# Kernel tuning notes

Measured on AMD Instinct MI355X. Metric: run time of the kernel, lower is better.

Reference implementation:

```python
import jax, jax.numpy as jnp
import numpy as np

B, T, C = 1, 2048, 1024
H = 16
HD = C // H
BLOCK = 2048
NEG = float('-inf')

def setup_inputs() -> dict:
    key = jax.random.key(0)
    ks = jax.random.split(key, 6)
    x = jax.random.normal(ks[0], (B, T, C), dtype=jnp.float32)
    cumulative_scores = jax.random.normal(ks[1], (B, T), dtype=jnp.float32) * 0.1
    padding_mask = jnp.ones((B, T), dtype=jnp.float32)
    token_index = jax.random.randint(ks[2], (B, T), 0, BLOCK).astype(jnp.int64)
    w_attn = jax.random.normal(ks[3], (C, 3 * C), dtype=jnp.float32) * (1.0 / np.sqrt(C))
    b_attn = jnp.zeros((3 * C,), dtype=jnp.float32)
    w_proj = jax.random.normal(ks[4], (C, C), dtype=jnp.float32) * (1.0 / np.sqrt(C))
    b_proj = jnp.zeros((C,), dtype=jnp.float32)
    return dict(x=x, cumulative_scores=cumulative_scores, padding_mask=padding_mask,
                token_index=token_index, w_attn=w_attn, b_attn=b_attn,
                w_proj=w_proj, b_proj=b_proj)

def _rotate_half(z):
    z1, z2 = z[..., : z.shape[-1] // 2], z[..., z.shape[-1] // 2 :]
    return jnp.concatenate((-z2, z1), axis=-1)

def reference(x, cumulative_scores, padding_mask, token_index, w_attn, b_attn, w_proj, b_proj):
    # fused QKV projection
    qkv = x @ w_attn + b_attn                      # (B,T,3C)
    q, k, v = jnp.split(qkv, 3, axis=2)
    q = q.reshape(B, T, H, HD).transpose(0, 2, 1, 3)  # (B,H,T,HD)
    k = k.reshape(B, T, H, HD).transpose(0, 2, 1, 3)
    v = v.reshape(B, T, H, HD).transpose(0, 2, 1, 3)

    # dynamic per-token RoPE positions: global token counts (original scatter
    # broadcasts indices over batch, so counts are global across all batches)
    cnt = jnp.zeros((BLOCK,), jnp.float32).at[token_index.reshape(-1)].add(1.0)
    per_tok = (1.0 / (cnt + 1e-10))[token_index]       # (B,T)
    partial = jnp.cumsum(per_tok, axis=-1)             # (B,T) fractional positions

    inv_freq = 1.0 / (10000.0 ** (jnp.arange(0, HD, 2, dtype=jnp.float32) / HD))
    freqs = partial[..., None] * inv_freq              # (B,T,HD/2)
    emb = jnp.concatenate((freqs, freqs), axis=-1)     # (B,T,HD)
    cos = jnp.cos(emb)[:, None]                        # (B,1,T,HD)
    sin = jnp.sin(emb)[:, None]
    q = q * cos + _rotate_half(q) * sin
    k = k * cos + _rotate_half(k) * sin

    # 'fork' plan: overwrite last channel
    q = q.at[..., -1].set(1.0)
    k = k.at[..., -1].set(jnp.broadcast_to(cumulative_scores[:, None, :], (B, H, T)))

    # additive causal + padding mask (B,T,T)
    causal = jnp.where(jnp.tril(jnp.ones((T, T), jnp.bool_)), 0.0, NEG)
    pm = jnp.take_along_axis(padding_mask, token_index, axis=1)     # (B,T)
    outer = pm[:, :, None] * pm[:, None, :]
    pad_add = jnp.where(outer.astype(jnp.bool_), 0.0, NEG)
    mask = causal[None, :, :] + pad_add                              # (B,T,T)

    # scale v by exp(cumulative_scores)
    v = v * jnp.exp(cumulative_scores)[:, None, :, None]

    scores = jnp.einsum('bhqd,bhkd->bhqk', q, k) / np.sqrt(HD) + mask[:, None]
    probs = jax.nn.softmax(scores, axis=-1)
    y = jnp.einsum('bhqk,bhkd->bhqd', probs, v)        # (B,H,T,HD)
    y = y.transpose(0, 2, 1, 3).reshape(B, T, C)
    return y @ w_proj + b_proj
```

## Files before the change

### kernel.cpp

```cpp
#include <hip/hip_runtime.h>
#include <math.h>

#define T 2048
#define C 1024
#define H 16
#define HD 64
#define N3 (3*C)
#define NBLOCK 2048

typedef __attribute__((ext_vector_type(8))) short bf16x8;
typedef __attribute__((ext_vector_type(4))) float f32x4;

#define MFMA16(a, b, c) __builtin_amdgcn_mfma_f32_16x16x32_bf16((a), (b), (c), 0, 0, 0)

__device__ inline short f2bf(float f) {
    unsigned u; __builtin_memcpy(&u, &f, 4);
    unsigned r = (u + 0x7fffu + ((u >> 16) & 1u)) >> 16;
    return (short)r;
}
__device__ inline float bf2f(short s) {
    unsigned u = ((unsigned)(unsigned short)s) << 16;
    float f; __builtin_memcpy(&f, &u, 4);
    return f;
}

__device__ inline void gload_lds16(const void* g, void* l) {
    __builtin_amdgcn_global_load_lds((const __attribute__((address_space(1))) unsigned int*)g,
                                     (__attribute__((address_space(3))) unsigned int*)l,
                                     16, 0, 0);
}

__global__ __launch_bounds__(256) void pre_kernel(const float* __restrict__ x,
                                                  const float* __restrict__ w_attn,
                                                  const float* __restrict__ w_proj,
                                                  const int* __restrict__ tok,
                                                  const float* __restrict__ padmask,
                                                  short* __restrict__ xb,
                                                  short* __restrict__ wabT,
                                                  short* __restrict__ wpbT,
                                                  float* __restrict__ partial,
                                                  float* __restrict__ pm_tok) {
    int bid = blockIdx.x;
    int tid = threadIdx.x;
    if (bid == 3072) {
        __shared__ float cntS[NBLOCK];
        __shared__ float sums[256];
        #pragma unroll
        for (int j = 0; j < 8; ++j) cntS[tid * 8 + j] = 0.0f;
        __syncthreads();
        int tk[8];
        #pragma unroll
        for (int j = 0; j < 8; ++j) {
            tk[j] = tok[tid * 8 + j];
            atomicAdd(&cntS[tk[j]], 1.0f);
        }
        __syncthreads();
        float vals[8];
        float s = 0.0f;
        #pragma unroll
        for (int j = 0; j < 8; ++j) {
            s += 1.0f / (cntS[tk[j]] + 1e-10f);
            vals[j] = s;
            pm_tok[tid * 8 + j] = padmask[tk[j]];
        }
        sums[tid] = s;
        __syncthreads();
        for (int off = 1; off < 256; off <<= 1) {
            float v = (tid >= off) ? sums[tid - off] : 0.0f;
            __syncthreads();
            sums[tid] += v;
            __syncthreads();
        }
        float offset = (tid > 0) ? sums[tid - 1] : 0.0f;
        #pragma unroll
        for (int j = 0; j < 8; ++j) partial[tid * 8 + j] = offset + vals[j];
        return;
    }
    if (bid < 2048) {
        int i = bid * 1024 + tid * 4;
        float4 v = *(const float4*)(x + i);
        short4 o;
        o.x = f2bf(v.x); o.y = f2bf(v.y); o.z = f2bf(v.z); o.w = f2bf(v.w);
        *(short4*)(xb + i) = o;
        return;
    }
    __shared__ float S[64][65];
    const float* in; short* out; int Kd, Nd, bx, by;
    if (bid < 2816) {
        int b = bid - 2048;
        bx = b % 48; by = b / 48;
        in = w_attn; out = wabT; Kd = C; Nd = N3;
    } else {
        int b = bid - 2816;
        bx = b % 16; by = b / 16;
        in = w_proj; out = wpbT; Kd = C; Nd = C;
    }
    int n0 = bx * 64, k0 = by * 64;
    #pragma unroll
    for (int i = 0; i < 16; ++i) {
        int lin = tid + i * 256;
        int r = lin >> 6, c = lin & 63;
        S[r][c] = in[(size_t)(k0 + r) * Nd + n0 + c];
    }
    __syncthreads();
    #pragma unroll
    for (int i = 0; i < 16; ++i) {
        int lin = tid + i * 256;
        int rn = lin >> 6, ck = lin & 63;
        out[(size_t)(n0 + rn) * Kd + k0 + ck] = f2bf(S[ck][rn]);
    }
}

template <int OUT_BF16, int EPI>
__global__ __launch_bounds__(256) void gemm_bt64(const short* __restrict__ A,
                                                 const short* __restrict__ Bt,
                                                 const float* __restrict__ bias,
                                                 void* __restrict__ Cout,
                                                 int M, int N, int K,
                                                 const float* __restrict__ partial,
                                                 const float* __restrict__ cumsc,
                                                 const float* __restrict__ pm_tok,
                                                 short* __restrict__ vbT) {
    __shared__ alignas(16) short As[2][64 * 32];
    __shared__ alignas(16) short Bs[2][128 * 32];
    int tid = threadIdx.x;
    int nwg = gridDim.x * gridDim.y;
    int bidl = blockIdx.y * gridDim.x + blockIdx.x;
    int swz = (bidl & 7) * (nwg >> 3) + (bidl >> 3);
    int m0 = (swz / gridDim.x) * 64, n0 = (swz % gridDim.x) * 128;
    int w = tid >> 6, l = tid & 63;
    int wm = (w >> 1) * 32, wn = (w & 1) * 64;
    int lq = l & 15, g = l >> 4;
    int prow = l >> 2, pcol = (l & 3) * 8;
    f32x4 acc[2][4] = {};
    for (int k0 = 0; k0 < K; k0 += 64) {
        #pragma unroll
        for (int hf = 0; hf < 2; ++hf) {
            int kk = k0 + hf * 32;
            int rowA = w * 16 + prow;
            gload_lds16(A + (size_t)(m0 + rowA) * K + kk + pcol, As[hf] + w * 512);
            #pragma unroll
            for (int i = 0; i < 2; ++i) {
                int c = w * 2 + i;
                int row = c * 16 + prow;
                gload_lds16(Bt + (size_t)(n0 + row) * K + kk + pcol, Bs[hf] + c * 512);
            }
        }
        __syncthreads();
        #pragma unroll
        for (int hf = 0; hf < 2; ++hf) {
            bf16x8 af[2], bfr[4];
            #pragma unroll
            for (int f = 0; f < 2; ++f)
                af[f] = *(const bf16x8*)(As[hf] + (wm + f * 16 + lq) * 32 + g * 8);
            #pragma unroll
            for (int j = 0; j < 4; ++j)
                bfr[j] = *(const bf16x8*)(Bs[hf] + (wn + j * 16 + lq) * 32 + g * 8);
            #pragma unroll
            for (int fi = 0; fi < 2; ++fi)
                #pragma unroll
                for (int fj = 0; fj < 4; ++fj)
                    acc[fi][fj] = MFMA16(af[fi], bfr[fj], acc[fi][fj]);
        }
        __syncthreads();
    }

    if (EPI == 0) {
        #pragma unroll
        for (int fi = 0; fi < 2; ++fi)
            #pragma unroll
            for (int fj = 0; fj < 4; ++fj)
                #pragma unroll
                for (int r = 0; r < 4; ++r) {
                    int m = m0 + wm + fi * 16 + g * 4 + r;
                    int n = n0 + wn + fj * 16 + lq;
                    float v = acc[fi][fj][r] + bias[n];
                    if (OUT_BF16) ((short*)Cout)[(size_t)m * N + n] = f2bf(v);
                    else          ((float*)Cout)[(size_t)m * N + n] = v;
                }
    } else {
        short* Cb = (short*)Cout;
        int cb = n0 + wn;
        int section = cb >> 10;
        float b0 = bias[cb + lq],      b1 = bias[cb + 16 + lq];
        float b2 = bias[cb + 32 + lq], b3 = bias[cb + 48 + lq];
        if (section < 2) {
            bool isQ = (section == 0);
            float inv0 = exp2f(-(float)lq * (13.287712379549449f / 32.0f));
            float inv1 = exp2f(-(float)(lq + 16) * (13.287712379549449f / 32.0f));
            #pragma unroll
            for (int fi = 0; fi < 2; ++fi)
                #pragma unroll
                for (int r = 0; r < 4; ++r) {
                    int trow = m0 + wm + fi * 16 + g * 4 + r;
                    float pt = partial[trow];
                    float sn0, cs0, sn1, cs1;
                    __sincosf(pt * inv0, &sn0, &cs0);
                    __sincosf(pt * inv1, &sn1, &cs1);
                    float a0 = acc[fi][0][r] + b0;
                    float a1 = acc[fi][1][r] + b1;
                    float a2 = acc[fi][2][r] + b2;
                    float a3 = acc[fi][3][r] + b3;
                    float lo0 = a0 * cs0 - a2 * sn0;
                    float hi0 = a2 * cs0 + a0 * sn0;
                    float lo1 = a1 * cs1 - a3 * sn1;
                    float hi1 = a3 * cs1 + a1 * sn1;
                    if (lq == 15) {
                        float pm = pm_tok[trow];
                        hi1 = isQ ? ((pm != 0.0f) ? 1.0f : 0.0f)
                                  : ((pm != 0.0f) ? cumsc[trow] : -1e20f);
                    }
                    size_t base = (size_t)trow * N3 + cb;
                    Cb[base + lq]      = f2bf(lo0);
                    Cb[base + 16 + lq] = f2bf(lo1);
                    Cb[base + 32 + lq] = f2bf(hi0);
                    Cb[base + 48 + lq] = f2bf(hi1);
                }
        } else {
            int h = (cb - 2 * C) >> 6;
            #pragma unroll
            for (int fi = 0; fi < 2; ++fi) {
                int tb = m0 + wm + fi * 16 + g * 4;
                float ef[4];
                #pragma unroll
                for (int r = 0; r < 4; ++r) ef[r] = __expf(cumsc[tb + r]);
                #pragma unroll
                for (int fj = 0; fj < 4; ++fj) {
                    int d = fj * 16 + lq;
                    float bv = (fj == 0) ? b0 : (fj == 1) ? b1 : (fj == 2) ? b2 : b3;
                    short4 o;
                    o.x = f2bf((acc[fi][fj][0] + bv) * ef[0]);
                    o.y = f2bf((acc[fi][fj][1] + bv) * ef[1]);
                    o.z = f2bf((acc[fi][fj][2] + bv) * ef[2]);
                    o.w = f2bf((acc[fi][fj][3] + bv) * ef[3]);
                    *(short4*)(vbT + (size_t)(h * 64 + d) * T + tb) = o;
                }
            }
        }
    }
}

__global__ __launch_bounds__(256) void attn_flash(const short* __restrict__ qkvb,
                                                  const short* __restrict__ vbT,
                                                  short* __restrict__ yb) {
    __shared__ alignas(16) short Kt[2][64 * 64];
    __shared__ alignas(16) short Vt[2][64 * 64];
    __shared__ alignas(16) short Ps[4][16][72];

    int b = blockIdx.x;
    int h, qt;
    if (b < 256) { h = b & 15; qt = 31 - (b >> 4); }
    else         { int c2 = b - 256; h = c2 & 15; qt = c2 >> 4; }
    int tid = threadIdx.x;
    int w = tid >> 6, l = tid & 63;
    int lq = l & 15, g = l >> 4;
    int qrl = w * 16 + lq;

    const short* qbase = qkvb + (size_t)(qt * 64 + qrl) * N3 + h * 64;
    bf16x8 qf0 = *(const bf16x8*)(qbase + g * 8);
    bf16x8 qf1 = *(const bf16x8*)(qbase + 32 + g * 8);

    f32x4 accO[4] = {};
    float lsum = 0.0f;

    int srow = tid >> 3, scol = (tid & 7) * 8;
    const short* kgb = qkvb + C + h * 64 + scol;
    const short* vgb = vbT + (size_t)(h * 64) * T + scol;
    int wb0 = srow * 128 + ((scol * 2) ^ ((srow & 7) << 4));
    int wb1 = (srow + 32) * 128 + ((scol * 2) ^ ((srow & 7) << 4));

    auto do_tile = [&](int cur, bool masked) {
        const char* Kc = (const char*)Kt[cur];
        const char* Vc = (const char*)Vt[cur];
        f32x4 s[4] = {};
        __builtin_amdgcn_s_setprio(1);
        #pragma unroll
        for (int f = 0; f < 4; ++f) {
            int row = f * 16 + lq;
            const char* kr_ = Kc + row * 128;
            int sw = (row & 7) << 4;
            bf16x8 a0 = *(const bf16x8*)(kr_ + ((g * 16) ^ sw));
            bf16x8 a1 = *(const bf16x8*)(kr_ + ((64 + g * 16) ^ sw));
            s[f] = MFMA16(a0, qf0, s[f]);
            s[f] = MFMA16(a1, qf1, s[f]);
        }
        __builtin_amdgcn_s_setprio(0);
        float p[16];
        #pragma unroll
        for (int f = 0; f < 4; ++f)
            #pragma unroll
            for (int r = 0; r < 4; ++r) {
                float sv = s[f][r] * 0.125f;
                if (masked) {
                    int kl = f * 16 + g * 4 + r;
                    sv = (kl > qrl) ? -INFINITY : sv;
                }
                float pv = __expf(sv);
                p[f * 4 + r] = pv;
                lsum += pv;
            }
        #pragma unroll
        for (int f = 0; f < 4; ++f) {
            unsigned u0, u1;
            asm("v_cvt_pk_bf16_f32 %0, %1, %2" : "=v"(u0) : "v"(p[f * 4 + 0]), "v"(p[f * 4 + 1]));
            asm("v_cvt_pk_bf16_f32 %0, %1, %2" : "=v"(u1) : "v"(p[f * 4 + 2]), "v"(p[f * 4 + 3]));
            uint2 uu; uu.x = u0; uu.y = u1;
            *(uint2*)&Ps[w][lq][f * 16 + g * 4] = uu;
        }
        __builtin_amdgcn_s_setprio(1);
        #pragma unroll
        for (int kh = 0; kh < 2; ++kh) {
            bf16x8 pa = *(const bf16x8*)&Ps[w][lq][kh * 32 + g * 8];
            #pragma unroll
            for (int f = 0; f < 4; ++f) {
                int vrow = f * 16 + lq;
                const char* vr_ = Vc + vrow * 128;
                bf16x8 vb = *(const bf16x8*)(vr_ + (((kh * 32 + g * 8) * 2) ^ ((vrow & 7) << 4)));
                accO[f] = MFMA16(pa, vb, accO[f]);
            }
        }
        __builtin_amdgcn_s_setprio(0);
    };

    uint4 kr0 = *(const uint4*)(kgb + (size_t)srow * N3);
    uint4 kr1 = *(const uint4*)(kgb + (size_t)(srow + 32) * N3);
    uint4 vr0 = *(const uint4*)(vgb + (size_t)srow * T);
    uint4 vr1 = *(const uint4*)(vgb + (size_t)(srow + 32) * T);
    *(uint4*)((char*)Kt[0] + wb0) = kr0;
    *(uint4*)((char*)Kt[0] + wb1) = kr1;
    *(uint4*)((char*)Vt[0] + wb0) = vr0;
    *(uint4*)((char*)Vt[0] + wb1) = vr1;
    __syncthreads();

    for (int t = 0; t < qt; ++t) {
        int kn = (t + 1) * 64;
        kr0 = *(const uint4*)(kgb + (size_t)(kn + srow) * N3);
        kr1 = *(const uint4*)(kgb + (size_t)(kn + srow + 32) * N3);
        vr0 = *(const uint4*)(vgb + (size_t)srow * T + kn);
        vr1 = *(const uint4*)(vgb + (size_t)(srow + 32) * T + kn);

        do_tile(t & 1, false);

        int nxt = (t & 1) ^ 1;
        *(uint4*)((char*)Kt[nxt] + wb0) = kr0;
        *(uint4*)((char*)Kt[nxt] + wb1) = kr1;
        *(uint4*)((char*)Vt[nxt] + wb0) = vr0;
        *(uint4*)((char*)Vt[nxt] + wb1) = vr1;
        __syncthreads();
    }
    do_tile(qt & 1, true);

    lsum += __shfl_xor(lsum, 16);
    lsum += __shfl_xor(lsum, 32);
    float linv_own = 1.0f / lsum;
    float li[4];
    #pragma unroll
    for (int r = 0; r < 4; ++r) li[r] = __shfl(linv_own, g * 4 + r);

    #pragma unroll
    for (int f = 0; f < 4; ++f)
        #pragma unroll
        for (int r = 0; r < 4; ++r) {
            int trow = qt * 64 + w * 16 + g * 4 + r;
            yb[(size_t)trow * C + h * 64 + f * 16 + lq] = f2bf(accO[f][r] * li[r]);
        }
}

extern "C" void kernel_launch(void* const* d_in, const int* in_sizes, int n_in,
                              void* d_out, int out_size, void* d_ws, size_t ws_size,
                              hipStream_t stream) {
    const float* x       = (const float*)d_in[0];
    const float* cumsc   = (const float*)d_in[1];
    const float* padmask = (const float*)d_in[2];
    const int*   tok     = (const int*)d_in[3];
    const float* w_attn  = (const float*)d_in[4];
    const float* b_attn  = (const float*)d_in[5];
    const float* w_proj  = (const float*)d_in[6];
    const float* b_proj  = (const float*)d_in[7];
    float* out = (float*)d_out;

    float* part   = (float*)d_ws;
    float* pm_tok = part + 2048;
    short* xb     = (short*)(pm_tok + 2048);
    short* wabT   = xb + (size_t)T * C;
    short* wpbT   = wabT + (size_t)N3 * C;
    short* qkvb   = wpbT + (size_t)C * C;
    short* vbT    = qkvb + (size_t)T * N3;
    short* yb     = vbT + (size_t)C * T;

    pre_kernel<<<3073, 256, 0, stream>>>(x, w_attn, w_proj, tok, padmask,
                                         xb, wabT, wpbT, part, pm_tok);
    gemm_bt64<1, 1><<<dim3(N3 / 128, T / 64), 256, 0, stream>>>(
        xb, wabT, b_attn, qkvb, T, N3, C, part, cumsc, pm_tok, vbT);
    attn_flash<<<512, 256, 0, stream>>>(qkvb, vbT, yb);
    gemm_bt64<0, 0><<<dim3(C / 128, T / 64), 256, 0, stream>>>(
        yb, wpbT, b_proj, out, T, C, C, nullptr, nullptr, nullptr, nullptr);
}
```

Baseline: 83.29 us.

## Split long causal attention rows across two blocks and combine partials

Query tiles 16-31 now have their key range split into two blocks (tiles 0-16 and 17-qt). Each half writes unnormalized fp32 partial outputs and row sums to workspace, and a new combine kernel adds them, normalizes, and writes bf16. This balances per-block work under the causal mask and raises block count from 512 to 768. The cost is an extra kernel launch plus fp32 partial writes and reads. The split relies on there being no running max, which matches the existing unnormalized softmax.

```diff
diff --git a/kernel.cpp b/kernel.cpp
--- a/kernel.cpp
+++ b/kernel.cpp
@@ -242,21 +242,27 @@
 
 __global__ __launch_bounds__(256) void attn_flash(const short* __restrict__ qkvb,
                                                   const short* __restrict__ vbT,
-                                                  short* __restrict__ yb) {
+                                                  short* __restrict__ yb,
+                                                  float* __restrict__ Opart,
+                                                  float* __restrict__ Lpart) {
     __shared__ alignas(16) short Kt[2][64 * 64];
     __shared__ alignas(16) short Vt[2][64 * 64];
     __shared__ alignas(16) short Ps[4][16][72];
 
     int b = blockIdx.x;
-    int h, qt;
-    if (b < 256) { h = b & 15; qt = 31 - (b >> 4); }
-    else         { int c2 = b - 256; h = c2 & 15; qt = c2 >> 4; }
+    int h, qt, t0, t1, mode;
+    if (b < 256)      { h = b & 15; qt = 16 + (b >> 4); t0 = 0;  t1 = 16; mode = 1; }
+    else if (b < 512) { int c = b - 256; h = c & 15; qt = 31 - (c >> 4); t0 = 17; t1 = qt; mode = 2; }
+    else              { int c = b - 512; h = c & 15; qt = c >> 4; t0 = 0; t1 = qt; mode = 0; }
+    int nt = t1 - t0 + 1;
+
     int tid = threadIdx.x;
     int w = tid >> 6, l = tid & 63;
     int lq = l & 15, g = l >> 4;
     int qrl = w * 16 + lq;
-
-    const short* qbase = qkvb + (size_t)(qt * 64 + qrl) * N3 + h * 64;
+    int qrow = qt * 64 + qrl;
+
+    const short* qbase = qkvb + (size_t)qrow * N3 + h * 64;
     bf16x8 qf0 = *(const bf16x8*)(qbase + g * 8);
     bf16x8 qf1 = *(const bf16x8*)(qbase + 32 + g * 8);
 
@@ -269,9 +275,24 @@
     int wb0 = srow * 128 + ((scol * 2) ^ ((srow & 7) << 4));
     int wb1 = (srow + 32) * 128 + ((scol * 2) ^ ((srow & 7) << 4));
 
-    auto do_tile = [&](int cur, bool masked) {
-        const char* Kc = (const char*)Kt[cur];
-        const char* Vc = (const char*)Vt[cur];
+    uint4 kr0, kr1, vr0, vr1;
+    auto stageRegs = [&](int tile) {
+        int kb = tile * 64;
+        kr0 = *(const uint4*)(kgb + (size_t)(kb + srow) * N3);
+        kr1 = *(const uint4*)(kgb + (size_t)(kb + srow + 32) * N3);
+        vr0 = *(const uint4*)(vgb + (size_t)srow * T + kb);
+        vr1 = *(const uint4*)(vgb + (size_t)(srow + 32) * T + kb);
+    };
+    auto writeLds = [&](int buf) {
+        *(uint4*)((char*)Kt[buf] + wb0) = kr0;
+        *(uint4*)((char*)Kt[buf] + wb1) = kr1;
+        *(uint4*)((char*)Vt[buf] + wb0) = vr0;
+        *(uint4*)((char*)Vt[buf] + wb1) = vr1;
+    };
+
+    auto do_tile = [&](int buf, bool masked) {
+        const char* Kc = (const char*)Kt[buf];
+        const char* Vc = (const char*)Vt[buf];
         f32x4 s[4] = {};
         __builtin_amdgcn_s_setprio(1);
         #pragma unroll
@@ -322,48 +343,74 @@
         __builtin_amdgcn_s_setprio(0);
     };
 
-    uint4 kr0 = *(const uint4*)(kgb + (size_t)srow * N3);
-    uint4 kr1 = *(const uint4*)(kgb + (size_t)(srow + 32) * N3);
-    uint4 vr0 = *(const uint4*)(vgb + (size_t)srow * T);
-    uint4 vr1 = *(const uint4*)(vgb + (size_t)(srow + 32) * T);
-    *(uint4*)((char*)Kt[0] + wb0) = kr0;
-    *(uint4*)((char*)Kt[0] + wb1) = kr1;
-    *(uint4*)((char*)Vt[0] + wb0) = vr0;
-    *(uint4*)((char*)Vt[0] + wb1) = vr1;
+    if (nt > 0) { stageRegs(t0); writeLds(0); }
     __syncthreads();
 
-    for (int t = 0; t < qt; ++t) {
-        int kn = (t + 1) * 64;
-        kr0 = *(const uint4*)(kgb + (size_t)(kn + srow) * N3);
-        kr1 = *(const uint4*)(kgb + (size_t)(kn + srow + 32) * N3);
-        vr0 = *(const uint4*)(vgb + (size_t)srow * T + kn);
-        vr1 = *(const uint4*)(vgb + (size_t)(srow + 32) * T + kn);
-
-        do_tile(t & 1, false);
-
-        int nxt = (t & 1) ^ 1;
-        *(uint4*)((char*)Kt[nxt] + wb0) = kr0;
-        *(uint4*)((char*)Kt[nxt] + wb1) = kr1;
-        *(uint4*)((char*)Vt[nxt] + wb0) = vr0;
-        *(uint4*)((char*)Vt[nxt] + wb1) = vr1;
-        __syncthreads();
-    }
-    do_tile(qt & 1, true);
+    for (int j = 0; j < nt; ++j) {
+        int t = t0 + j;
+        bool pf = (j + 1 < nt);
+        if (pf) stageRegs(t + 1);
+        do_tile(j & 1, t == qt);
+        if (pf) writeLds((j & 1) ^ 1);
+        __syncthreads();
+    }
 
     lsum += __shfl_xor(lsum, 16);
     lsum += __shfl_xor(lsum, 32);
-    float linv_own = 1.0f / lsum;
-    float li[4];
+
+    if (mode == 0) {
+        float linv_own = 1.0f / lsum;
+        float li[4];
+        #pragma unroll
+        for (int r = 0; r < 4; ++r) li[r] = __shfl(linv_own, g * 4 + r);
+        #pragma unroll
+        for (int f = 0; f < 4; ++f)
+            #pragma unroll
+            for (int r = 0; r < 4; ++r) {
+                int trow = qt * 64 + w * 16 + g * 4 + r;
+                yb[(size_t)trow * C + h * 64 + f * 16 + lq] = f2bf(accO[f][r] * li[r]);
+            }
+    } else {
+        int kh = mode - 1;
+        int slab = h * 16 + (qt - 16);
+        float* Ob = Opart + ((size_t)kh * 256 + slab) * 4096;
+        #pragma unroll
+        for (int f = 0; f < 4; ++f)
+            #pragma unroll
+            for (int r = 0; r < 4; ++r)
+                Ob[(w * 16 + g * 4 + r) * 64 + f * 16 + lq] = accO[f][r];
+        if (g == 0) Lpart[((size_t)kh * 256 + slab) * 64 + w * 16 + lq] = lsum;
+    }
+}
+
+__global__ __launch_bounds__(256) void attn_combine(const float* __restrict__ Opart,
+                                                    const float* __restrict__ Lpart,
+                                                    short* __restrict__ yb) {
+    __shared__ float linvS[64];
+    int s = blockIdx.x;
+    int h = s >> 4, qt = 16 + (s & 15);
+    int tid = threadIdx.x;
+    if (tid < 64)
+        linvS[tid] = 1.0f / (Lpart[(size_t)s * 64 + tid] + Lpart[(size_t)(256 + s) * 64 + tid]);
+    __syncthreads();
+    const float* O0 = Opart + (size_t)s * 4096;
+    const float* O1 = Opart + (size_t)(256 + s) * 4096;
     #pragma unroll
-    for (int r = 0; r < 4; ++r) li[r] = __shfl(linv_own, g * 4 + r);
-
-    #pragma unroll
-    for (int f = 0; f < 4; ++f)
-        #pragma unroll
-        for (int r = 0; r < 4; ++r) {
-            int trow = qt * 64 + w * 16 + g * 4 + r;
-            yb[(size_t)trow * C + h * 64 + f * 16 + lq] = f2bf(accO[f][r] * li[r]);
-        }
+    for (int e = 0; e < 4; ++e) {
+        int idx = (tid * 4 + e * 1024);
+        int base = tid * 4 + e * 1024;
+        float4 a = *(const float4*)(O0 + base);
+        float4 c = *(const float4*)(O1 + base);
+        int q = base >> 6, d = base & 63;
+        float li = linvS[q];
+        short4 o;
+        o.x = f2bf((a.x + c.x) * li);
+        o.y = f2bf((a.y + c.y) * li);
+        o.z = f2bf((a.z + c.z) * li);
+        o.w = f2bf((a.w + c.w) * li);
+        *(short4*)(yb + (size_t)(qt * 64 + q) * C + h * 64 + d) = o;
+        (void)idx;
+    }
 }
 
 extern "C" void kernel_launch(void* const* d_in, const int* in_sizes, int n_in,
@@ -381,7 +428,9 @@
 
     float* part   = (float*)d_ws;
     float* pm_tok = part + 2048;
-    short* xb     = (short*)(pm_tok + 2048);
+    float* Opart  = pm_tok + 2048;
+    float* Lpart  = Opart + (size_t)2 * 256 * 4096;
+    short* xb     = (short*)(Lpart + 2 * 256 * 64);
     short* wabT   = xb + (size_t)T * C;
     short* wpbT   = wabT + (size_t)N3 * C;
     short* qkvb   = wpbT + (size_t)C * C;
@@ -392,7 +441,8 @@
                                          xb, wabT, wpbT, part, pm_tok);
     gemm_bt64<1, 1><<<dim3(N3 / 128, T / 64), 256, 0, stream>>>(
         xb, wabT, b_attn, qkvb, T, N3, C, part, cumsc, pm_tok, vbT);
-    attn_flash<<<512, 256, 0, stream>>>(qkvb, vbT, yb);
+    attn_flash<<<768, 256, 0, stream>>>(qkvb, vbT, yb, Opart, Lpart);
+    attn_combine<<<256, 256, 0, stream>>>(Opart, Lpart, yb);
     gemm_bt64<0, 0><<<dim3(C / 128, T / 64), 256, 0, stream>>>(
         yb, wpbT, b_proj, out, T, C, C, nullptr, nullptr, nullptr, nullptr);
 }
```

Result: faster. 81.57 us (-2.1%).
